# Kernel tuning notes

Hardware: AMD Instinct MI355X
Metric: run time of the kernel (lower is better)

The kernel has to match this reference:

```python
import jax, jax.numpy as jnp
import numpy as np

B, T, V, E, U = 256, 512, 20000, 128, 128


def setup_inputs() -> dict:
    key = jax.random.key(0)
    k = jax.random.split(key, 7)
    tokens = jax.random.randint(k[0], (B, T), 0, V)
    emb_table = jax.random.normal(k[1], (V, E), jnp.float32) * 0.05
    kernel = jax.random.normal(k[2], (E, 4 * U), jnp.float32) * 0.05
    recurrent_kernel = jax.random.normal(k[3], (U, 4 * U), jnp.float32) * 0.05
    # Keras default: unit_forget_bias -> forget-gate bias = 1, others 0 (gate order i,f,c,o)
    bias = jnp.concatenate([jnp.zeros(U), jnp.ones(U), jnp.zeros(2 * U)]).astype(jnp.float32)
    dense_w = jax.random.normal(k[4], (U, 1), jnp.float32) * 0.05
    dense_b = jnp.zeros((1,), jnp.float32)
    return {"tokens": tokens, "emb_table": emb_table, "kernel": kernel,
            "recurrent_kernel": recurrent_kernel, "bias": bias,
            "dense_w": dense_w, "dense_b": dense_b}


def reference(tokens, emb_table, kernel, recurrent_kernel, bias, dense_w, dense_b):
    # Embedding lookup: [B,T] -> [B,T,E]
    x = emb_table[tokens]
    # Precompute input projections for all timesteps: [B,T,4U]
    zx = jnp.einsum('bte,eg->btg', x, kernel) + bias

    def step(carry, z_t):
        h, c = carry
        z = z_t + h @ recurrent_kernel          # [B,4U]
        i, f, g, o = jnp.split(z, 4, axis=-1)   # Keras gate order i,f,c,o
        i = jax.nn.sigmoid(i)
        f = jax.nn.sigmoid(f)
        g = jnp.tanh(g)
        o = jax.nn.sigmoid(o)
        c = f * c + i * g
        h = o * jnp.tanh(c)
        return (h, c), None

    h0 = jnp.zeros((tokens.shape[0], U), zx.dtype)
    c0 = jnp.zeros((tokens.shape[0], U), zx.dtype)
    (h_final, _), _ = jax.lax.scan(step, (h0, c0), jnp.swapaxes(zx, 0, 1))
    # Dense sigmoid head: [B,1]
    return jax.nn.sigmoid(h_final @ dense_w + dense_b)
```

## Files before the change

kernel.cpp:

```cpp
#include <hip/hip_runtime.h>
#include <hip/hip_bf16.h>

#define BB 256
#define TT 512
#define VV 20000
#define EE 128
#define UU 128
#define G4 512

typedef _Float16 f16x8 __attribute__((ext_vector_type(8)));
typedef float    f32x4 __attribute__((ext_vector_type(4)));

__device__ __forceinline__ float sigmoid_f(float x) {
    float e = __expf(-x);
    return __builtin_amdgcn_rcpf(1.0f + e);
}
__device__ __forceinline__ float tanh_f(float x) {
    float e = __expf(2.0f * x);
    return 1.0f - 2.0f * __builtin_amdgcn_rcpf(e + 1.0f);
}

__global__ __launch_bounds__(512, 2) void proj_kernel(
    const float* __restrict__ emb, const float* __restrict__ wk,
    const float* __restrict__ bias, float* __restrict__ P2) {
    const int tid = threadIdx.x;
    const int g   = tid & 3;
    const int u   = tid >> 2;
    const int col = g * 128 + u;
    const int v0  = blockIdx.x * 16;

    __shared__ float elds[16 * EE];
    ((float4*)elds)[tid] = ((const float4*)(emb + (size_t)v0 * EE))[tid];
    __syncthreads();

    float bcol = bias[col];
    float acc[16];
#pragma unroll
    for (int r = 0; r < 16; ++r) acc[r] = bcol;

    const float4* elds4 = (const float4*)elds;
    for (int e0 = 0; e0 < EE; e0 += 4) {
        float k0 = wk[(e0 + 0) * G4 + col];
        float k1 = wk[(e0 + 1) * G4 + col];
        float k2 = wk[(e0 + 2) * G4 + col];
        float k3 = wk[(e0 + 3) * G4 + col];
#pragma unroll
        for (int r = 0; r < 16; ++r) {
            float4 ev = elds4[r * 32 + (e0 >> 2)];
            acc[r] = fmaf(ev.x, k0, acc[r]);
            acc[r] = fmaf(ev.y, k1, acc[r]);
            acc[r] = fmaf(ev.z, k2, acc[r]);
            acc[r] = fmaf(ev.w, k3, acc[r]);
        }
    }
#pragma unroll
    for (int r = 0; r < 16; ++r)
        P2[(size_t)(v0 + r) * G4 + tid] = acc[r];
}

__global__ __launch_bounds__(512, 2) void lstm_kernel(
    const int* __restrict__ tokens, const float* __restrict__ rk,
    const float* __restrict__ P2, const float* __restrict__ dense_w,
    const float* __restrict__ dense_b, float* __restrict__ out) {
    const int tid = threadIdx.x;
    const int w   = tid >> 6;
    const int l   = tid & 63;
    const int j   = l & 15;
    const int kq  = l >> 4;
    const int b   = blockIdx.x;
    const int ucol = 16 * w + j;

    __shared__ __align__(16) _Float16 hbuf[2][UU];
    __shared__ int   tokLDS[TT];
    __shared__ float red[8];

    f16x8 bf[4][4];
#pragma unroll
    for (int kt = 0; kt < 4; ++kt) {
#pragma unroll
        for (int g = 0; g < 4; ++g) {
            f16x8 v;
#pragma unroll
            for (int i = 0; i < 8; ++i) {
                v[i] = (_Float16)rk[(size_t)(32 * kt + 8 * kq + i) * G4
                                    + g * 128 + ucol];
            }
            bf[kt][g] = v;
        }
    }

    const int* trow = tokens + (size_t)b * TT;
    tokLDS[tid] = trow[tid];
    if (tid < UU) hbuf[0][tid] = (_Float16)0.f;
    float c_state = 0.f, hv = 0.f;

    const float4* Pc4 = (const float4*)(P2 + (size_t)ucol * 4);
    float4 pf[4];
#pragma unroll
    for (int s = 0; s < 4; ++s) pf[s] = Pc4[(size_t)trow[s] * 128];
    __syncthreads();

    const f32x4 cz = {0.f, 0.f, 0.f, 0.f};

    for (int t = 0; t < TT; t += 4) {
#pragma unroll
        for (int s = 0; s < 4; ++s) {
            int tki  = t + s + 4; if (tki > TT - 1) tki = TT - 1;
            int vtok = tokLDS[tki];

            f16x8 af[4];
#pragma unroll
            for (int kt = 0; kt < 4; ++kt)
                af[kt] = *(const f16x8*)&hbuf[s & 1][32 * kt + 8 * kq];

            float4 pnew = Pc4[(size_t)vtok * 128];

            f32x4 accA[4], accB[4];
#pragma unroll
            for (int g = 0; g < 4; ++g) {
                accA[g] = __builtin_amdgcn_mfma_f32_16x16x32_f16(af[0], bf[0][g], cz, 0, 0, 0);
                accB[g] = __builtin_amdgcn_mfma_f32_16x16x32_f16(af[2], bf[2][g], cz, 0, 0, 0);
            }
#pragma unroll
            for (int g = 0; g < 4; ++g) {
                accA[g] = __builtin_amdgcn_mfma_f32_16x16x32_f16(af[1], bf[1][g], accA[g], 0, 0, 0);
                accB[g] = __builtin_amdgcn_mfma_f32_16x16x32_f16(af[3], bf[3][g], accB[g], 0, 0, 0);
            }

            float z0 = accA[0][0] + accB[0][0] + pf[s].x;
            float z1 = accA[1][0] + accB[1][0] + pf[s].y;
            float z2 = accA[2][0] + accB[2][0] + pf[s].z;
            float z3 = accA[3][0] + accB[3][0] + pf[s].w;

            float gi = sigmoid_f(z0);
            float gf = sigmoid_f(z1);
            float gg = tanh_f(z2);
            float go = sigmoid_f(z3);
            c_state = fmaf(gf, c_state, gi * gg);
            hv      = go * tanh_f(c_state);

            if (kq == 0) hbuf[(s + 1) & 1][ucol] = (_Float16)hv;
            pf[s] = pnew;

            asm volatile("s_waitcnt lgkmcnt(0)" ::: "memory");
            __builtin_amdgcn_s_barrier();
        }
    }

    float val = (kq == 0) ? hv * dense_w[ucol] : 0.f;
#pragma unroll
    for (int off = 32; off > 0; off >>= 1) val += __shfl_xor(val, off, 64);
    if (l == 0) red[w] = val;
    __syncthreads();
    if (tid == 0) {
        float sum = dense_b[0];
#pragma unroll
        for (int i = 0; i < 8; ++i) sum += red[i];
        out[b] = sigmoid_f(sum);
    }
}

extern "C" void kernel_launch(void* const* d_in, const int* in_sizes, int n_in,
                              void* d_out, int out_size, void* d_ws, size_t ws_size,
                              hipStream_t stream) {
    const int*   tokens = (const int*)  d_in[0];
    const float* emb    = (const float*)d_in[1];
    const float* wk     = (const float*)d_in[2];
    const float* rk     = (const float*)d_in[3];
    const float* bias   = (const float*)d_in[4];
    const float* dw     = (const float*)d_in[5];
    const float* db     = (const float*)d_in[6];
    float* out = (float*)d_out;
    float* P2  = (float*)d_ws;

    proj_kernel<<<VV / 16, 512, 0, stream>>>(emb, wk, bias, P2);
    lstm_kernel<<<BB, 512, 0, stream>>>(tokens, rk, P2, dw, db, out);
}
```

Baseline: 289.8 us.

## Interleave two batch rows per LSTM block and split gate activations across lanes

Each LSTM workgroup now advances two independent batch recurrences per timestep, interleaving the MFMA chains and gate math of row B with row A. The aim is to hide the serial latency of each step. Gate nonlinearities are spread so each kq lane evaluates one gate, with tanh rewritten as 2·sigmoid(2x)−1. The four gate values are then exchanged through an LDS buffer, which cuts transcendental work per lane. The grid is halved to 128 blocks with launch bounds relaxed to 1, so half the CUs sit idle. The P2 prefetch also shifts to per-lane scalar loads driven by readfirstlane token indices.

```diff
diff --git a/kernel.cpp b/kernel.cpp
--- a/kernel.cpp
+++ b/kernel.cpp
@@ -7,6 +7,7 @@
 #define EE 128
 #define UU 128
 #define G4 512
+#define ROWS 2
 
 typedef _Float16 f16x8 __attribute__((ext_vector_type(8)));
 typedef float    f32x4 __attribute__((ext_vector_type(4)));
@@ -58,7 +59,7 @@
         P2[(size_t)(v0 + r) * G4 + tid] = acc[r];
 }
 
-__global__ __launch_bounds__(512, 2) void lstm_kernel(
+__global__ __launch_bounds__(512, 1) void lstm_kernel(
     const int* __restrict__ tokens, const float* __restrict__ rk,
     const float* __restrict__ P2, const float* __restrict__ dense_w,
     const float* __restrict__ dense_b, float* __restrict__ out) {
@@ -67,12 +68,13 @@
     const int l   = tid & 63;
     const int j   = l & 15;
     const int kq  = l >> 4;
-    const int b   = blockIdx.x;
+    const int rb  = blockIdx.x * ROWS;
     const int ucol = 16 * w + j;
 
-    __shared__ __align__(16) _Float16 hbuf[2][UU];
-    __shared__ int   tokLDS[TT];
-    __shared__ float red[8];
+    __shared__ __align__(16) _Float16 hbuf[ROWS][2][UU];
+    __shared__ __align__(16) float    gbuf[ROWS][G4];
+    __shared__ int tokLDS[ROWS][TT + 8];
+    __shared__ float red[ROWS][8];
 
     f16x8 bf[4][4];
 #pragma unroll
@@ -89,74 +91,119 @@
         }
     }
 
-    const int* trow = tokens + (size_t)b * TT;
-    tokLDS[tid] = trow[tid];
-    if (tid < UU) hbuf[0][tid] = (_Float16)0.f;
-    float c_state = 0.f, hv = 0.f;
-
-    const float4* Pc4 = (const float4*)(P2 + (size_t)ucol * 4);
-    float4 pf[4];
-#pragma unroll
-    for (int s = 0; s < 4; ++s) pf[s] = Pc4[(size_t)trow[s] * 128];
+#pragma unroll
+    for (int r = 0; r < ROWS; ++r) {
+        tokLDS[r][tid] = tokens[(size_t)(rb + r) * TT + tid];
+        if (tid < 8) tokLDS[r][TT + tid] = tokens[(size_t)(rb + r) * TT + TT - 1];
+    }
+    if (tid < UU) { hbuf[0][0][tid] = (_Float16)0.f; hbuf[1][0][tid] = (_Float16)0.f; }
+
+    const int pOff = ucol * 4 + kq;
+    float c0 = 0.f, c1 = 0.f, hv0 = 0.f, hv1 = 0.f;
+
+    const int* tr0 = tokens + (size_t)rb * TT;
+    const int* tr1 = tokens + (size_t)(rb + 1) * TT;
+    float pA0 = P2[(size_t)tr0[0] * G4 + pOff];
+    float pB0 = P2[(size_t)tr1[0] * G4 + pOff];
+    float pA1 = P2[(size_t)tr0[1] * G4 + pOff];
+    float pB1 = P2[(size_t)tr1[1] * G4 + pOff];
     __syncthreads();
 
     const f32x4 cz = {0.f, 0.f, 0.f, 0.f};
 
-    for (int t = 0; t < TT; t += 4) {
-#pragma unroll
-        for (int s = 0; s < 4; ++s) {
-            int tki  = t + s + 4; if (tki > TT - 1) tki = TT - 1;
-            int vtok = tokLDS[tki];
-
-            f16x8 af[4];
-#pragma unroll
-            for (int kt = 0; kt < 4; ++kt)
-                af[kt] = *(const f16x8*)&hbuf[s & 1][32 * kt + 8 * kq];
-
-            float4 pnew = Pc4[(size_t)vtok * 128];
-
-            f32x4 accA[4], accB[4];
-#pragma unroll
-            for (int g = 0; g < 4; ++g) {
-                accA[g] = __builtin_amdgcn_mfma_f32_16x16x32_f16(af[0], bf[0][g], cz, 0, 0, 0);
-                accB[g] = __builtin_amdgcn_mfma_f32_16x16x32_f16(af[2], bf[2][g], cz, 0, 0, 0);
-            }
-#pragma unroll
-            for (int g = 0; g < 4; ++g) {
-                accA[g] = __builtin_amdgcn_mfma_f32_16x16x32_f16(af[1], bf[1][g], accA[g], 0, 0, 0);
-                accB[g] = __builtin_amdgcn_mfma_f32_16x16x32_f16(af[3], bf[3][g], accB[g], 0, 0, 0);
-            }
-
-            float z0 = accA[0][0] + accB[0][0] + pf[s].x;
-            float z1 = accA[1][0] + accB[1][0] + pf[s].y;
-            float z2 = accA[2][0] + accB[2][0] + pf[s].z;
-            float z3 = accA[3][0] + accB[3][0] + pf[s].w;
-
-            float gi = sigmoid_f(z0);
-            float gf = sigmoid_f(z1);
-            float gg = tanh_f(z2);
-            float go = sigmoid_f(z3);
-            c_state = fmaf(gf, c_state, gi * gg);
-            hv      = go * tanh_f(c_state);
-
-            if (kq == 0) hbuf[(s + 1) & 1][ucol] = (_Float16)hv;
-            pf[s] = pnew;
-
-            asm volatile("s_waitcnt lgkmcnt(0)" ::: "memory");
-            __builtin_amdgcn_s_barrier();
-        }
-    }
-
-    float val = (kq == 0) ? hv * dense_w[ucol] : 0.f;
-#pragma unroll
-    for (int off = 32; off > 0; off >>= 1) val += __shfl_xor(val, off, 64);
-    if (l == 0) red[w] = val;
+#define LSTM_STEP(PAR, PA, PB)                                                 \
+    {                                                                          \
+        const int ia = t + (PAR) + 2;                                          \
+        int vA = tokLDS[0][ia];                                                \
+        int vB = tokLDS[1][ia];                                                \
+        float curA = (PA), curB = (PB);                                        \
+        int sA = __builtin_amdgcn_readfirstlane(vA);                           \
+        int sB = __builtin_amdgcn_readfirstlane(vB);                           \
+        (PA) = P2[(size_t)sA * G4 + pOff];             \
+        (PB) = P2[(size_t)sB * G4 + pOff];                                     \
+        f16x8 afA[4], afB[4];                                                  \
+        _Pragma("unroll")                                                      \
+        for (int kt = 0; kt < 4; ++kt) {                                       \
+            afA[kt] = *(const f16x8*)&hbuf[0][PAR][32 * kt + 8 * kq];          \
+            afB[kt] = *(const f16x8*)&hbuf[1][PAR][32 * kt + 8 * kq];          \
+        }                                                                      \
+                                   \
+        f32x4 accA[4];                                                         \
+        _Pragma("unroll")                                                      \
+        for (int g = 0; g < 4; ++g) {                                          \
+            f32x4 a = __builtin_amdgcn_mfma_f32_16x16x32_f16(afA[0], bf[0][g], cz, 0, 0, 0); \
+            a = __builtin_amdgcn_mfma_f32_16x16x32_f16(afA[1], bf[1][g], a, 0, 0, 0); \
+            a = __builtin_amdgcn_mfma_f32_16x16x32_f16(afA[2], bf[2][g], a, 0, 0, 0); \
+            a = __builtin_amdgcn_mfma_f32_16x16x32_f16(afA[3], bf[3][g], a, 0, 0, 0); \
+            accA[g] = a;                                                       \
+        }                                                                      \
+              \
+        {                                                                      \
+            float z0 = accA[0][0], z1 = accA[1][0], z2 = accA[2][0], z3 = accA[3][0]; \
+            float zlo = (kq & 1) ? z1 : z0;                                    \
+            float zhi = (kq & 1) ? z3 : z2;                                    \
+            float zl  = ((kq & 2) ? zhi : zlo) + curA;                         \
+            float xs  = (kq == 2) ? zl + zl : zl;                              \
+            float sg  = sigmoid_f(xs);                                         \
+            float av  = (kq == 2) ? fmaf(2.f, sg, -1.f) : sg;                  \
+            gbuf[0][ucol * 4 + kq] = av;                                       \
+        }                                                                      \
+                                   \
+        f32x4 accB[4];                                                         \
+        _Pragma("unroll")                                                      \
+        for (int g = 0; g < 4; ++g) {                                          \
+            f32x4 a = __builtin_amdgcn_mfma_f32_16x16x32_f16(afB[0], bf[0][g], cz, 0, 0, 0); \
+            a = __builtin_amdgcn_mfma_f32_16x16x32_f16(afB[1], bf[1][g], a, 0, 0, 0); \
+            a = __builtin_amdgcn_mfma_f32_16x16x32_f16(afB[2], bf[2][g], a, 0, 0, 0); \
+            a = __builtin_amdgcn_mfma_f32_16x16x32_f16(afB[3], bf[3][g], a, 0, 0, 0); \
+            accB[g] = a;                                                       \
+        }                                                                      \
+         \
+        {                                                                      \
+            float4 g4 = *(const float4*)&gbuf[0][ucol * 4];                    \
+            c0  = fmaf(g4.y, c0, g4.x * g4.z);                                 \
+            hv0 = g4.w * tanh_f(c0);                                           \
+            if (kq == 0) hbuf[0][(PAR) ^ 1][ucol] = (_Float16)hv0;             \
+        }                                                                      \
+                                 \
+        {                                                                      \
+            float z0 = accB[0][0], z1 = accB[1][0], z2 = accB[2][0], z3 = accB[3][0]; \
+            float zlo = (kq & 1) ? z1 : z0;                                    \
+            float zhi = (kq & 1) ? z3 : z2;                                    \
+            float zl  = ((kq & 2) ? zhi : zlo) + curB;                         \
+            float xs  = (kq == 2) ? zl + zl : zl;                              \
+            float sg  = sigmoid_f(xs);                                         \
+            float av  = (kq == 2) ? fmaf(2.f, sg, -1.f) : sg;                  \
+            gbuf[1][ucol * 4 + kq] = av;                                       \
+            float4 g4 = *(const float4*)&gbuf[1][ucol * 4];                    \
+            c1  = fmaf(g4.y, c1, g4.x * g4.z);                                 \
+            hv1 = g4.w * tanh_f(c1);                                           \
+            if (kq == 1) hbuf[1][(PAR) ^ 1][ucol] = (_Float16)hv1;             \
+        }                                                                      \
+        asm volatile("s_waitcnt lgkmcnt(0)" ::: "memory");                     \
+        __builtin_amdgcn_s_barrier();                                          \
+    }
+
+    for (int t = 0; t < TT; t += 2) {
+        LSTM_STEP(0, pA0, pB0)
+        LSTM_STEP(1, pA1, pB1)
+    }
+#undef LSTM_STEP
+
+    float v0 = (kq == 0) ? hv0 * dense_w[ucol] : 0.f;
+    float v1 = (kq == 0) ? hv1 * dense_w[ucol] : 0.f;
+#pragma unroll
+    for (int off = 32; off > 0; off >>= 1) {
+        v0 += __shfl_xor(v0, off, 64);
+        v1 += __shfl_xor(v1, off, 64);
+    }
+    if (l == 0) { red[0][w] = v0; red[1][w] = v1; }
     __syncthreads();
-    if (tid == 0) {
-        float sum = dense_b[0];
-#pragma unroll
-        for (int i = 0; i < 8; ++i) sum += red[i];
-        out[b] = sigmoid_f(sum);
+    if (tid < ROWS) {
+        float s = dense_b[0];
+#pragma unroll
+        for (int i = 0; i < 8; ++i) s += red[tid][i];
+        out[rb + tid] = sigmoid_f(s);
     }
 }
 
@@ -174,5 +221,5 @@
     float* P2  = (float*)d_ws;
 
     proj_kernel<<<VV / 16, 512, 0, stream>>>(emb, wk, bias, P2);
-    lstm_kernel<<<BB, 512, 0, stream>>>(tokens, rk, P2, dw, db, out);
-}
+    lstm_kernel<<<BB / ROWS, 512, 0, stream>>>(tokens, rk, P2, dw, db, out);
+}
```

Measured after the change: 497.6 us. +71.7%, slower.

## Replace MFMA recurrent matvec with fdot2 per-thread dot products and DPP reductions

Applied to the files above, without the earlier changes.

The recurrent h·W product moves off MFMA. Each thread now holds half2 weight slices for its 32-wide K chunk across all four gates, computes them with v_dot2 instructions, and reduces the partial sums across quads with DPP moves. Each quad lane then evaluates one gate activation, and the four results are broadcast over DPP. This avoids the MFMA issue latency and the zero-padded 16x16 tile work on a batch-1 matvec, and the prefetch depth drops from 4 steps to 2. The cost is more VALU instructions and higher register pressure per thread.

```diff
diff --git a/kernel.cpp b/kernel.cpp
--- a/kernel.cpp
+++ b/kernel.cpp
@@ -8,8 +8,7 @@
 #define UU 128
 #define G4 512
 
-typedef _Float16 f16x8 __attribute__((ext_vector_type(8)));
-typedef float    f32x4 __attribute__((ext_vector_type(4)));
+typedef _Float16 half2v __attribute__((ext_vector_type(2)));
 
 __device__ __forceinline__ float sigmoid_f(float x) {
     float e = __expf(-x);
@@ -18,6 +17,21 @@
 __device__ __forceinline__ float tanh_f(float x) {
     float e = __expf(2.0f * x);
     return 1.0f - 2.0f * __builtin_amdgcn_rcpf(e + 1.0f);
+}
+
+__device__ __forceinline__ float dot2f(half2v a, half2v b, float c) {
+    return __builtin_amdgcn_fdot2(a, b, c, false);
+}
+
+__device__ __forceinline__ float dpp_q(float v, int pat) {
+    switch (pat) {
+        case 0xB1: return __int_as_float(__builtin_amdgcn_mov_dpp(__float_as_int(v), 0xB1, 0xF, 0xF, true));
+        case 0x4E: return __int_as_float(__builtin_amdgcn_mov_dpp(__float_as_int(v), 0x4E, 0xF, 0xF, true));
+        case 0x00: return __int_as_float(__builtin_amdgcn_mov_dpp(__float_as_int(v), 0x00, 0xF, 0xF, true));
+        case 0x55: return __int_as_float(__builtin_amdgcn_mov_dpp(__float_as_int(v), 0x55, 0xF, 0xF, true));
+        case 0xAA: return __int_as_float(__builtin_amdgcn_mov_dpp(__float_as_int(v), 0xAA, 0xF, 0xF, true));
+        default:   return __int_as_float(__builtin_amdgcn_mov_dpp(__float_as_int(v), 0xFF, 0xF, 0xF, true));
+    }
 }
 
 __global__ __launch_bounds__(512, 2) void proj_kernel(
@@ -58,105 +72,128 @@
         P2[(size_t)(v0 + r) * G4 + tid] = acc[r];
 }
 
-__global__ __launch_bounds__(512, 2) void lstm_kernel(
+__global__ __launch_bounds__(512) __attribute__((amdgpu_waves_per_eu(2, 2)))
+void lstm_kernel(
     const int* __restrict__ tokens, const float* __restrict__ rk,
     const float* __restrict__ P2, const float* __restrict__ dense_w,
     const float* __restrict__ dense_b, float* __restrict__ out) {
     const int tid = threadIdx.x;
-    const int w   = tid >> 6;
-    const int l   = tid & 63;
-    const int j   = l & 15;
-    const int kq  = l >> 4;
+    const int u   = tid >> 2;
+    const int q   = tid & 3;
     const int b   = blockIdx.x;
-    const int ucol = 16 * w + j;
-
-    __shared__ __align__(16) _Float16 hbuf[2][UU];
-    __shared__ int   tokLDS[TT];
+
+    __shared__ __align__(16) _Float16 hh[2][UU];
+    __shared__ int   tokLDS[TT + 4];
     __shared__ float red[8];
 
-    f16x8 bf[4][4];
-#pragma unroll
-    for (int kt = 0; kt < 4; ++kt) {
-#pragma unroll
-        for (int g = 0; g < 4; ++g) {
-            f16x8 v;
-#pragma unroll
-            for (int i = 0; i < 8; ++i) {
-                v[i] = (_Float16)rk[(size_t)(32 * kt + 8 * kq + i) * G4
-                                    + g * 128 + ucol];
-            }
-            bf[kt][g] = v;
+    half2v wgt[4][16];
+    const float* rkb = rk + (size_t)(32 * q) * G4;
+#pragma unroll
+    for (int g = 0; g < 4; ++g) {
+        const int c = g * 128 + u;
+#pragma unroll
+        for (int p = 0; p < 16; ++p) {
+            half2v hw;
+            hw.x = (_Float16)rkb[(2 * p + 0) * G4 + c];
+            hw.y = (_Float16)rkb[(2 * p + 1) * G4 + c];
+            wgt[g][p] = hw;
         }
     }
 
     const int* trow = tokens + (size_t)b * TT;
     tokLDS[tid] = trow[tid];
-    if (tid < UU) hbuf[0][tid] = (_Float16)0.f;
+    if (tid < 4) tokLDS[TT + tid] = trow[TT - 1];
+    if (tid < UU) hh[0][tid] = (_Float16)0.f;
+
+    const int pOff = 4 * u + q;
     float c_state = 0.f, hv = 0.f;
-
-    const float4* Pc4 = (const float4*)(P2 + (size_t)ucol * 4);
-    float4 pf[4];
-#pragma unroll
-    for (int s = 0; s < 4; ++s) pf[s] = Pc4[(size_t)trow[s] * 128];
+    float pf0 = P2[(size_t)trow[0] * G4 + pOff];
+    float pf1 = P2[(size_t)trow[1] * G4 + pOff];
     __syncthreads();
 
-    const f32x4 cz = {0.f, 0.f, 0.f, 0.f};
-
-    for (int t = 0; t < TT; t += 4) {
-#pragma unroll
-        for (int s = 0; s < 4; ++s) {
-            int tki  = t + s + 4; if (tki > TT - 1) tki = TT - 1;
-            int vtok = tokLDS[tki];
-
-            f16x8 af[4];
-#pragma unroll
-            for (int kt = 0; kt < 4; ++kt)
-                af[kt] = *(const f16x8*)&hbuf[s & 1][32 * kt + 8 * kq];
-
-            float4 pnew = Pc4[(size_t)vtok * 128];
-
-            f32x4 accA[4], accB[4];
-#pragma unroll
-            for (int g = 0; g < 4; ++g) {
-                accA[g] = __builtin_amdgcn_mfma_f32_16x16x32_f16(af[0], bf[0][g], cz, 0, 0, 0);
-                accB[g] = __builtin_amdgcn_mfma_f32_16x16x32_f16(af[2], bf[2][g], cz, 0, 0, 0);
-            }
-#pragma unroll
-            for (int g = 0; g < 4; ++g) {
-                accA[g] = __builtin_amdgcn_mfma_f32_16x16x32_f16(af[1], bf[1][g], accA[g], 0, 0, 0);
-                accB[g] = __builtin_amdgcn_mfma_f32_16x16x32_f16(af[3], bf[3][g], accB[g], 0, 0, 0);
-            }
-
-            float z0 = accA[0][0] + accB[0][0] + pf[s].x;
-            float z1 = accA[1][0] + accB[1][0] + pf[s].y;
-            float z2 = accA[2][0] + accB[2][0] + pf[s].z;
-            float z3 = accA[3][0] + accB[3][0] + pf[s].w;
-
-            float gi = sigmoid_f(z0);
-            float gf = sigmoid_f(z1);
-            float gg = tanh_f(z2);
-            float go = sigmoid_f(z3);
-            c_state = fmaf(gf, c_state, gi * gg);
-            hv      = go * tanh_f(c_state);
-
-            if (kq == 0) hbuf[(s + 1) & 1][ucol] = (_Float16)hv;
-            pf[s] = pnew;
-
-            asm volatile("s_waitcnt lgkmcnt(0)" ::: "memory");
-            __builtin_amdgcn_s_barrier();
-        }
-    }
-
-    float val = (kq == 0) ? hv * dense_w[ucol] : 0.f;
+#define LSTEP(PAR, PF)                                                        \
+    {                                                                         \
+        int vtok = tokLDS[t + (PAR) + 2];                                     \
+        float pcur = (PF);                        \
+        (PF) = P2[(size_t)vtok * G4 + pOff];          \
+        const int4* hrow = (const int4*)&hh[PAR][32 * q];                     \
+        int4 hA = hrow[0], hB = hrow[1], hC = hrow[2], hD = hrow[3];          \
+        half2v h2[16];                                                        \
+        h2[0]  = __builtin_bit_cast(half2v, hA.x);                            \
+        h2[1]  = __builtin_bit_cast(half2v, hA.y);                            \
+        h2[2]  = __builtin_bit_cast(half2v, hA.z);                            \
+        h2[3]  = __builtin_bit_cast(half2v, hA.w);                            \
+        h2[4]  = __builtin_bit_cast(half2v, hB.x);                            \
+        h2[5]  = __builtin_bit_cast(half2v, hB.y);                            \
+        h2[6]  = __builtin_bit_cast(half2v, hB.z);                            \
+        h2[7]  = __builtin_bit_cast(half2v, hB.w);                            \
+        h2[8]  = __builtin_bit_cast(half2v, hC.x);                            \
+        h2[9]  = __builtin_bit_cast(half2v, hC.y);                            \
+        h2[10] = __builtin_bit_cast(half2v, hC.z);                            \
+        h2[11] = __builtin_bit_cast(half2v, hC.w);                            \
+        h2[12] = __builtin_bit_cast(half2v, hD.x);                            \
+        h2[13] = __builtin_bit_cast(half2v, hD.y);                            \
+        h2[14] = __builtin_bit_cast(half2v, hD.z);                            \
+        h2[15] = __builtin_bit_cast(half2v, hD.w);                            \
+          \
+        float acc0[4], acc1[4];                                               \
+        _Pragma("unroll")                                                     \
+        for (int g = 0; g < 4; ++g) {                                         \
+            acc0[g] = (q == g) ? pcur : 0.f;                                  \
+            acc1[g] = 0.f;                                                    \
+        }                                                                     \
+        _Pragma("unroll")                                                     \
+        for (int p = 0; p < 16; p += 2) {                                     \
+            _Pragma("unroll")                                                 \
+            for (int g = 0; g < 4; ++g) {                                     \
+                acc0[g] = dot2f(h2[p],     wgt[g][p],     acc0[g]);           \
+                acc1[g] = dot2f(h2[p + 1], wgt[g][p + 1], acc1[g]);           \
+            }                                                                 \
+        }                                                                     \
+                 \
+        float z0, z1, z2, z3;                                                 \
+        {                                                                     \
+            float s;                                                          \
+            s = acc0[0] + acc1[0]; s += dpp_q(s, 0xB1); s += dpp_q(s, 0x4E); z0 = s; \
+            s = acc0[1] + acc1[1]; s += dpp_q(s, 0xB1); s += dpp_q(s, 0x4E); z1 = s; \
+            s = acc0[2] + acc1[2]; s += dpp_q(s, 0xB1); s += dpp_q(s, 0x4E); z2 = s; \
+            s = acc0[3] + acc1[3]; s += dpp_q(s, 0xB1); s += dpp_q(s, 0x4E); z3 = s; \
+        }                                                                     \
+                                  \
+        float zlo = (q & 1) ? z1 : z0;                                        \
+        float zhi = (q & 1) ? z3 : z2;                                        \
+        float zq  = (q & 2) ? zhi : zlo;                                      \
+        float xs  = (q == 2) ? zq + zq : zq;                                  \
+        float sg  = sigmoid_f(xs);                                            \
+        float av  = (q == 2) ? fmaf(2.f, sg, -1.f) : sg;                      \
+                                     \
+        float ai = dpp_q(av, 0x00);                                           \
+        float af_ = dpp_q(av, 0x55);                                          \
+        float ag = dpp_q(av, 0xAA);                                           \
+        float ao = dpp_q(av, 0xFF);                                           \
+        c_state = fmaf(af_, c_state, ai * ag);                                \
+        hv      = ao * tanh_f(c_state);                                       \
+        if (q == 0) hh[(PAR) ^ 1][u] = (_Float16)hv;                          \
+        asm volatile("s_waitcnt lgkmcnt(0)" ::: "memory");                    \
+        __builtin_amdgcn_s_barrier();                                         \
+    }
+
+    for (int t = 0; t < TT; t += 2) {
+        LSTEP(0, pf0)
+        LSTEP(1, pf1)
+    }
+#undef LSTEP
+
+    float val = (q == 0) ? hv * dense_w[u] : 0.f;
 #pragma unroll
     for (int off = 32; off > 0; off >>= 1) val += __shfl_xor(val, off, 64);
-    if (l == 0) red[w] = val;
+    if ((tid & 63) == 0) red[tid >> 6] = val;
     __syncthreads();
     if (tid == 0) {
-        float sum = dense_b[0];
-#pragma unroll
-        for (int i = 0; i < 8; ++i) sum += red[i];
-        out[b] = sigmoid_f(sum);
+        float s = dense_b[0];
+#pragma unroll
+        for (int i = 0; i < 8; ++i) s += red[i];
+        out[b] = sigmoid_f(s);
     }
 }
 
```

After: 334.0 us. 1.15x slower.
